# Kernel optimization log

Hardware: AMD Instinct MI355X
Metric: run time of the kernel (lower is better)

## Reference

```python
import jax, jax.numpy as jnp
from jax import lax
import numpy as np

B, C, L, HOP = 16, 64, 16384, 256
KS = 3        # LVC / conv kernel size
DIL = 3       # static Conv1d dilation (init arg)
KL = L // HOP # kernel_length (number of conditioning frames)


def setup_inputs() -> dict:
    key = jax.random.key(0)
    k0, k1, k2, k3 = jax.random.split(key, 4)
    return {
        "hidden_states": jax.random.normal(k0, (B, C, L), jnp.float32),
        "kernel": jax.random.normal(k1, (B, C, 2 * C, KS, KL), jnp.float32) * 0.05,
        "bias": jax.random.normal(k2, (B, 2 * C, KL), jnp.float32) * 0.05,
        "conv_w": jax.random.normal(k3, (C, C, KS), jnp.float32) * 0.05,
        "conv_b": jnp.zeros((C,), jnp.float32),
        "hop_size": HOP,
    }


def _lvc(x, kernel, bias, hop_size):
    # location-variable convolution; forward() uses dilation=1 here
    b, c, length = x.shape
    _, _, out_ch, ksize, klen = kernel.shape
    pad = (ksize - 1) // 2
    xp = jnp.pad(x, ((0, 0), (0, 0), (pad, pad)))
    # sliding windows of size ksize, stride 1 -> (b, c, length, ksize)
    win = jnp.stack([xp[:, :, i:i + length] for i in range(ksize)], axis=-1)
    # split time into (kernel_length, hop_size) frames
    win = win.reshape(b, c, klen, hop_size, ksize)
    # per-frame conv kernel contraction
    o = jnp.einsum('bilsk,biokl->bols', win, kernel)  # (b, out_ch, klen, hop)
    o = o + bias[:, :, :, None]
    return o.reshape(b, out_ch, klen * hop_size)


def reference(hidden_states, kernel, bias, conv_w, conv_b, hop_size):
    slope = 0.2
    pad = DIL * (KS - 1) // 2
    residual = hidden_states
    h = jax.nn.leaky_relu(hidden_states, slope)
    h = lax.conv_general_dilated(
        h, conv_w, window_strides=(1,), padding=[(pad, pad)],
        rhs_dilation=(DIL,), dimension_numbers=('NCH', 'OIH', 'NCH'))
    h = h + conv_b[None, :, None]
    h = jax.nn.leaky_relu(h, slope)
    h = _lvc(h, kernel, bias, hop_size)
    c = residual.shape[1]
    h = jax.nn.sigmoid(h[:, :c, :]) * jnp.tanh(h[:, c:, :])  # GLU gate
    return residual + h
```

## Files before the change

kernel.cpp:

```cpp
#include <hip/hip_runtime.h>
#include <hip/hip_bf16.h>

#define TB 256

typedef __attribute__((ext_vector_type(8))) short short8;
typedef __attribute__((ext_vector_type(4))) unsigned int uint4v;
typedef __attribute__((ext_vector_type(4))) float f32x4;

#define KTF_BYTES 50331648ull
#define WS_NEED   (KTF_BYTES + 24576ull)

static __device__ __forceinline__ float lrelu(float v){ return v > 0.f ? v : 0.2f*v; }

static __device__ __forceinline__ unsigned int pack2(float lo, float hi){
    __hip_bfloat162 h = __float22bfloat162_rn(float2{lo, hi});
    unsigned int r;
    __builtin_memcpy(&r, &h, 4);
    return r;
}

static __device__ __forceinline__ float bf2f(unsigned int u16v){
    return __uint_as_float(u16v << 16);
}

static __device__ __forceinline__ float glu_gate(float a, float t){
    float sg = 1.0f / (1.0f + __expf(-a));
    float e  = __expf(-2.0f * t);
    float th = 2.0f / (1.0f + e) - 1.0f;
    return sg * th;
}


__global__ __launch_bounds__(256, 4)
void ktf_transpose(const float* __restrict__ kern, unsigned int* __restrict__ ktf)
{
    __shared__ unsigned int tl32[128 * 65];
    const int tid = threadIdx.x;
    const int blk = blockIdx.x;
    const int k   = blk % 3;
    const int ci2 = (blk / 3) % 32;
    const int b   = blk / 96;
    const int kk  = k*2 + (ci2 >> 4);
    const int hi  = (ci2 >> 2) & 3;
    const int jp  = ci2 & 3;

    const float* src0 = kern + (size_t)b*1572864 + (size_t)ci2*49152 + k*64;
    #pragma unroll
    for (int it = 0; it < 8; ++it) {
        int p = tid + it*TB;
        int oc = p >> 4, fq = p & 15;
        const float* s = src0 + oc*192 + fq*4;
        float4 v0 = *(const float4*)(s);
        float4 v1 = *(const float4*)(s + 24576);
        unsigned int* d = tl32 + oc*65 + fq*4;
        d[0] = pack2(v0.x, v1.x);
        d[1] = pack2(v0.y, v1.y);
        d[2] = pack2(v0.z, v1.z);
        d[3] = pack2(v0.w, v1.w);
    }
    __syncthreads();

    const int l = tid & 63, wv = tid >> 6;
    const int mt = l >> 3, lo2 = (2*l) & 15;
    const size_t obase = (size_t)((kk*4 + jp)*8 + mt)*64 + hi*16 + lo2;
    #pragma unroll
    for (int fi = 0; fi < 16; ++fi) {
        int f = wv*16 + fi;
        uint2 v;
        v.x = tl32[(2*l    )*65 + f];
        v.y = tl32[(2*l + 1)*65 + f];
        *(uint2*)(ktf + (size_t)(b*64 + f)*12288 + obase) = v;
    }
}

__global__ __launch_bounds__(256, 4)
void wf_prep(const float* __restrict__ conv_w, unsigned int* __restrict__ wf)
{
    int u = blockIdx.x*TB + threadIdx.x;
    int ln = u & 63, mt = (u >> 6) & 3, jp = (u >> 8) & 3, kk = u >> 10;
    int lo = ln & 15, hi = ln >> 4;
    int m  = mt*16 + lo;
    int k  = kk >> 1, ci = (kk & 1)*32 + hi*8 + jp*2;
    float a0 = conv_w[m*192 + ci*3 + k];
    float a1 = conv_w[m*192 + (ci + 1)*3 + k];
    wf[u] = pack2(a0, a1);
}

#define LDS_BYTES (36864 + 34816 + 512)

__global__ __launch_bounds__(512, 4)
void fused_kernel(const float* __restrict__ x,
                  const float* __restrict__ bias,
                  const float* __restrict__ conv_b,
                  const unsigned int* __restrict__ ktf,
                  const unsigned int* __restrict__ wf,
                  float* __restrict__ out)
{
    __shared__ char lds[LDS_BYTES];
    float* bias_lds = (float*)(lds + 71680);

    const int tid = threadIdx.x;
    const int blk = blockIdx.x;
    const int b = blk >> 6, f = blk & 63;
    const int t0 = f << 8;
    const int ln = tid & 63, wv = tid >> 6;
    const int lo = ln & 15, hi = ln >> 4;
    const int mt = wv & 3, nth = wv >> 2;

    {
        const int g = wv;
        const float* xb = x + ((size_t)b*64 + g*8) * 16384;
        const bool interior = (f > 0) & (f < 63);
        #pragma unroll
        for (int it = 0; it < 5; ++it) {
            if (it < 4 || ln < 32) {
                int p = ln + it*64;
                int t = t0 - 12 + p;
                float v[8];
                if (interior) {
                    #pragma unroll
                    for (int j = 0; j < 8; ++j) v[j] = xb[j*16384 + t];
                } else {
                    bool ok = (unsigned)t < 16384u;
                    #pragma unroll
                    for (int j = 0; j < 8; ++j) v[j] = ok ? xb[j*16384 + t] : 0.f;
                }
                unsigned int w0 = pack2(lrelu(v[0]), lrelu(v[1]));
                unsigned int w1 = pack2(lrelu(v[2]), lrelu(v[3]));
                unsigned int w2 = pack2(lrelu(v[4]), lrelu(v[5]));
                unsigned int w3 = pack2(lrelu(v[6]), lrelu(v[7]));
                int addr = (p*128 + g*16) ^ ((p & 7) << 4);
                *(uint4*)(lds + addr) = make_uint4(w0, w1, w2, w3);
            }
        }
        if (tid < 128) bias_lds[tid] = bias[(size_t)b*8192 + tid*64 + f];
    }
    __syncthreads();

    {
        uint4v aw[6];
        #pragma unroll
        for (int kk = 0; kk < 6; ++kk) {
            int w0 = kk*1024 + mt*64 + ln;
            aw[kk].x = wf[w0      ]; aw[kk].y = wf[w0 + 256];
            aw[kk].z = wf[w0 + 512]; aw[kk].w = wf[w0 + 768];
        }
        float4 cb4 = *(const float4*)(conv_b + mt*16 + hi*4);
        const int n0  = nth ? 9 : 0;
        const int cnt = nth ? 8 : 9;
        #pragma unroll 1
        for (int i = 0; i < cnt; ++i) {
            int nt = n0 + i;
            short8 bq[6];
            #pragma unroll
            for (int kk = 0; kk < 6; ++kk) {
                int row = nt*16 + lo + 3*(kk >> 1) + 1;
                int cib = (kk & 1)*32 + hi*8;
                int addr = (row*128 + cib*2) ^ ((row & 7) << 4);
                bq[kk] = *(const short8*)(lds + addr);
            }
            f32x4 acc = {0.f, 0.f, 0.f, 0.f};
            __builtin_amdgcn_s_setprio(1);
            #pragma unroll
            for (int kk = 0; kk < 6; ++kk)
                acc = __builtin_amdgcn_mfma_f32_16x16x32_bf16(
                        __builtin_bit_cast(short8, aw[kk]), bq[kk], acc, 0, 0, 0);
            __builtin_amdgcn_s_setprio(0);

            int pos = t0 + nt*16 + lo - 8;
            bool valid = (unsigned)pos < 16384u;
            unsigned int h01 = valid ? pack2(lrelu(acc[0] + cb4.x), lrelu(acc[1] + cb4.y)) : 0u;
            unsigned int h23 = valid ? pack2(lrelu(acc[2] + cb4.z), lrelu(acc[3] + cb4.w)) : 0u;

            int htrow = nt*16 + lo;
            int addr = 36864 + ((htrow*128 + (mt*16 + hi*4)*2) ^ ((htrow & 7) << 4));
            unsigned int* d = (unsigned int*)(lds + addr);
            d[0] = h01; d[1] = h23;
        }
    }
    __syncthreads();

    {
        const unsigned int* kp = ktf + (size_t)blk * 12288;
        uint4v am0[6], am1[6];
        #pragma unroll
        for (int kk = 0; kk < 6; ++kk) {
            int b0 = kk*2048 + mt*64 + ln;
            am0[kk].x = kp[b0      ]; am0[kk].y = kp[b0 +  512];
            am0[kk].z = kp[b0 + 1024]; am0[kk].w = kp[b0 + 1536];
            int b1 = b0 + 256;
            am1[kk].x = kp[b1      ]; am1[kk].y = kp[b1 +  512];
            am1[kk].z = kp[b1 + 1024]; am1[kk].w = kp[b1 + 1536];
        }
        float ba[4], bb[4];
        size_t rowbase[4];
        #pragma unroll
        for (int r = 0; r < 4; ++r) {
            int c = mt*16 + hi*4 + r;
            ba[r] = bias_lds[c];
            bb[r] = bias_lds[c + 64];
            rowbase[r] = (size_t)(b*64 + c)*16384 + t0 + lo;
        }

        #pragma unroll 1
        for (int i = 0; i < 8; ++i) {
            int nt = nth*8 + i;
            int s = nt*16 + lo;
            short8 bq[6];
            #pragma unroll
            for (int kk = 0; kk < 6; ++kk) {
                int row = s + (kk >> 1) + 7;
                int cib = (kk & 1)*32 + hi*8;
                int addr = 36864 + ((row*128 + cib*2) ^ ((row & 7) << 4));
                bq[kk] = *(const short8*)(lds + addr);
            }
            int p = s + 12;
            int raddr = (p*128 + (mt*16 + hi*4)*2) ^ ((p & 7) << 4);
            uint2 rv = *(const uint2*)(lds + raddr);

            f32x4 a0 = {0.f,0.f,0.f,0.f}, a1 = {0.f,0.f,0.f,0.f};
            __builtin_amdgcn_s_setprio(1);
            #pragma unroll
            for (int kk = 0; kk < 6; ++kk) {
                a0 = __builtin_amdgcn_mfma_f32_16x16x32_bf16(
                        __builtin_bit_cast(short8, am0[kk]), bq[kk], a0, 0, 0, 0);
                a1 = __builtin_amdgcn_mfma_f32_16x16x32_bf16(
                        __builtin_bit_cast(short8, am1[kk]), bq[kk], a1, 0, 0, 0);
            }
            __builtin_amdgcn_s_setprio(0);

            #pragma unroll
            for (int r = 0; r < 4; ++r) {
                unsigned int u = (r < 2 ? rv.x : rv.y) >> ((r & 1) * 16);
                float hv = bf2f(u & 0xFFFFu);
                float xr = hv > 0.f ? hv : 5.0f * hv;
                float g  = glu_gate(a0[r] + ba[r], a1[r] + bb[r]);
                out[rowbase[r] + nt*16] = xr + g;
            }
        }
    }
}

extern "C" void kernel_launch(void* const* d_in, const int* in_sizes, int n_in,
                              void* d_out, int out_size, void* d_ws, size_t ws_size,
                              hipStream_t stream)
{
    const float* x      = (const float*)d_in[0];
    const float* kern   = (const float*)d_in[1];
    const float* bias   = (const float*)d_in[2];
    const float* conv_b = (const float*)d_in[4];
    float* out = (float*)d_out;

    if (ws_size < WS_NEED) return;

    unsigned int* ktf = (unsigned int*)d_ws;
    unsigned int* wf  = (unsigned int*)((char*)d_ws + KTF_BYTES);

    wf_prep      <<<dim3(24),   dim3(TB), 0, stream>>>((const float*)d_in[3], wf);
    ktf_transpose<<<dim3(1536), dim3(TB), 0, stream>>>(kern, ktf);
    fused_kernel <<<dim3(1024), dim3(512), 0, stream>>>(x, bias, conv_b, ktf, wf, out);
    (void)in_sizes; (void)n_in; (void)out_size;
}
```

Measured before the change: 90.52 us.

## Overlap x, weight and LVC kernel loads; vectorize x fetch; cheapen GLU gate

```diff
diff --git a/kernel.cpp b/kernel.cpp
--- a/kernel.cpp
+++ b/kernel.cpp
@@ -24,10 +24,11 @@
 }
 
 static __device__ __forceinline__ float glu_gate(float a, float t){
-    float sg = 1.0f / (1.0f + __expf(-a));
-    float e  = __expf(-2.0f * t);
-    float th = 2.0f / (1.0f + e) - 1.0f;
-    return sg * th;
+    t = fminf(fmaxf(t, -10.f), 10.f);
+    float u = __expf(-a);
+    float v = __expf(2.0f * t);
+    float den = (1.0f + u) * (v + 1.0f);
+    return (v - 1.0f) * __builtin_amdgcn_rcpf(den);
 }
 
 
@@ -107,82 +108,70 @@
     const int lo = ln & 15, hi = ln >> 4;
     const int mt = wv & 3, nth = wv >> 2;
 
+    const int g = wv;
+    const float* xb = x + ((size_t)b*64 + g*8) * 16384;
+    float2 xv[24];
     {
-        const int g = wv;
-        const float* xb = x + ((size_t)b*64 + g*8) * 16384;
         const bool interior = (f > 0) & (f < 63);
-        #pragma unroll
-        for (int it = 0; it < 5; ++it) {
-            if (it < 4 || ln < 32) {
-                int p = ln + it*64;
-                int t = t0 - 12 + p;
-                float v[8];
-                if (interior) {
+        if (interior) {
+            #pragma unroll
+            for (int it = 0; it < 3; ++it) {
+                if (it < 2 || ln < 16) {
+                    int t = t0 - 12 + 2*ln + it*128;
                     #pragma unroll
-                    for (int j = 0; j < 8; ++j) v[j] = xb[j*16384 + t];
-                } else {
-                    bool ok = (unsigned)t < 16384u;
+                    for (int j = 0; j < 8; ++j)
+                        xv[it*8 + j] = *(const float2*)(xb + j*16384 + t);
+                }
+            }
+        } else {
+            #pragma unroll
+            for (int it = 0; it < 3; ++it) {
+                if (it < 2 || ln < 16) {
+                    int t = t0 - 12 + 2*ln + it*128;
                     #pragma unroll
-                    for (int j = 0; j < 8; ++j) v[j] = ok ? xb[j*16384 + t] : 0.f;
+                    for (int j = 0; j < 8; ++j) {
+                        float a = ((unsigned)t       < 16384u) ? xb[j*16384 + t    ] : 0.f;
+                        float c = ((unsigned)(t + 1) < 16384u) ? xb[j*16384 + t + 1] : 0.f;
+                        xv[it*8 + j] = make_float2(a, c);
+                    }
                 }
-                unsigned int w0 = pack2(lrelu(v[0]), lrelu(v[1]));
-                unsigned int w1 = pack2(lrelu(v[2]), lrelu(v[3]));
-                unsigned int w2 = pack2(lrelu(v[4]), lrelu(v[5]));
-                unsigned int w3 = pack2(lrelu(v[6]), lrelu(v[7]));
-                int addr = (p*128 + g*16) ^ ((p & 7) << 4);
-                *(uint4*)(lds + addr) = make_uint4(w0, w1, w2, w3);
             }
         }
         if (tid < 128) bias_lds[tid] = bias[(size_t)b*8192 + tid*64 + f];
     }
-    __syncthreads();
-
-    {
-        uint4v aw[6];
-        #pragma unroll
-        for (int kk = 0; kk < 6; ++kk) {
-            int w0 = kk*1024 + mt*64 + ln;
-            aw[kk].x = wf[w0      ]; aw[kk].y = wf[w0 + 256];
-            aw[kk].z = wf[w0 + 512]; aw[kk].w = wf[w0 + 768];
-        }
-        float4 cb4 = *(const float4*)(conv_b + mt*16 + hi*4);
-        const int n0  = nth ? 9 : 0;
-        const int cnt = nth ? 8 : 9;
-        #pragma unroll 1
-        for (int i = 0; i < cnt; ++i) {
-            int nt = n0 + i;
-            short8 bq[6];
-            #pragma unroll
-            for (int kk = 0; kk < 6; ++kk) {
-                int row = nt*16 + lo + 3*(kk >> 1) + 1;
-                int cib = (kk & 1)*32 + hi*8;
-                int addr = (row*128 + cib*2) ^ ((row & 7) << 4);
-                bq[kk] = *(const short8*)(lds + addr);
-            }
-            f32x4 acc = {0.f, 0.f, 0.f, 0.f};
-            __builtin_amdgcn_s_setprio(1);
-            #pragma unroll
-            for (int kk = 0; kk < 6; ++kk)
-                acc = __builtin_amdgcn_mfma_f32_16x16x32_bf16(
-                        __builtin_bit_cast(short8, aw[kk]), bq[kk], acc, 0, 0, 0);
-            __builtin_amdgcn_s_setprio(0);
-
-            int pos = t0 + nt*16 + lo - 8;
-            bool valid = (unsigned)pos < 16384u;
-            unsigned int h01 = valid ? pack2(lrelu(acc[0] + cb4.x), lrelu(acc[1] + cb4.y)) : 0u;
-            unsigned int h23 = valid ? pack2(lrelu(acc[2] + cb4.z), lrelu(acc[3] + cb4.w)) : 0u;
-
-            int htrow = nt*16 + lo;
-            int addr = 36864 + ((htrow*128 + (mt*16 + hi*4)*2) ^ ((htrow & 7) << 4));
-            unsigned int* d = (unsigned int*)(lds + addr);
-            d[0] = h01; d[1] = h23;
-        }
-    }
-    __syncthreads();
-
+    __builtin_amdgcn_sched_barrier(0);
+
+    uint4v aw[6];
+    #pragma unroll
+    for (int kk = 0; kk < 6; ++kk) {
+        int w0 = kk*1024 + mt*64 + ln;
+        aw[kk].x = wf[w0      ]; aw[kk].y = wf[w0 + 256];
+        aw[kk].z = wf[w0 + 512]; aw[kk].w = wf[w0 + 768];
+    }
+    __builtin_amdgcn_sched_barrier(0);
+
+    #pragma unroll
+    for (int it = 0; it < 3; ++it) {
+        if (it < 2 || ln < 16) {
+            int p0 = 2*ln + it*128;
+            unsigned int w0[4], w1[4];
+            #pragma unroll
+            for (int jq = 0; jq < 4; ++jq) {
+                float2 e0 = xv[it*8 + 2*jq], e1 = xv[it*8 + 2*jq + 1];
+                w0[jq] = pack2(lrelu(e0.x), lrelu(e1.x));
+                w1[jq] = pack2(lrelu(e0.y), lrelu(e1.y));
+            }
+            int a0 = ( p0     *128 + g*16) ^ (( p0      & 7) << 4);
+            int a1 = ((p0 + 1)*128 + g*16) ^ (((p0 + 1) & 7) << 4);
+            *(uint4*)(lds + a0) = make_uint4(w0[0], w0[1], w0[2], w0[3]);
+            *(uint4*)(lds + a1) = make_uint4(w1[0], w1[1], w1[2], w1[3]);
+        }
+    }
+    __builtin_amdgcn_sched_barrier(0);
+
+    uint4v am0[6], am1[6];
     {
         const unsigned int* kp = ktf + (size_t)blk * 12288;
-        uint4v am0[6], am1[6];
         #pragma unroll
         for (int kk = 0; kk < 6; ++kk) {
             int b0 = kk*2048 + mt*64 + ln;
@@ -192,6 +181,50 @@
             am1[kk].x = kp[b1      ]; am1[kk].y = kp[b1 +  512];
             am1[kk].z = kp[b1 + 1024]; am1[kk].w = kp[b1 + 1536];
         }
+    }
+    __syncthreads();
+
+    {
+        float4 cb4 = *(const float4*)(conv_b + mt*16 + hi*4);
+        const int n0  = nth ? 9 : 0;
+        const int cnt = nth ? 8 : 9;
+        int bqa[6];
+        #pragma unroll
+        for (int kk = 0; kk < 6; ++kk) {
+            int row = n0*16 + lo + 3*(kk >> 1) + 1;
+            int cib = (kk & 1)*32 + hi*8;
+            bqa[kk] = (row*128 + cib*2) ^ ((row & 7) << 4);
+        }
+        int hta  = 36864 + (((n0*16 + lo)*128 + (mt*16 + hi*4)*2) ^ ((lo & 7) << 4));
+        int pos  = t0 + n0*16 + lo - 8;
+        #pragma unroll 1
+        for (int i = 0; i < cnt; ++i) {
+            short8 bq[6];
+            #pragma unroll
+            for (int kk = 0; kk < 6; ++kk)
+                bq[kk] = *(const short8*)(lds + bqa[kk]);
+            f32x4 acc = {0.f, 0.f, 0.f, 0.f};
+            __builtin_amdgcn_s_setprio(1);
+            #pragma unroll
+            for (int kk = 0; kk < 6; ++kk)
+                acc = __builtin_amdgcn_mfma_f32_16x16x32_bf16(
+                        __builtin_bit_cast(short8, aw[kk]), bq[kk], acc, 0, 0, 0);
+            __builtin_amdgcn_s_setprio(0);
+
+            bool valid = (unsigned)pos < 16384u;
+            unsigned int h01 = valid ? pack2(lrelu(acc[0] + cb4.x), lrelu(acc[1] + cb4.y)) : 0u;
+            unsigned int h23 = valid ? pack2(lrelu(acc[2] + cb4.z), lrelu(acc[3] + cb4.w)) : 0u;
+            unsigned int* d = (unsigned int*)(lds + hta);
+            d[0] = h01; d[1] = h23;
+
+            #pragma unroll
+            for (int kk = 0; kk < 6; ++kk) bqa[kk] += 2048;
+            hta += 2048; pos += 16;
+        }
+    }
+    __syncthreads();
+
+    {
         float ba[4], bb[4];
         size_t rowbase[4];
         #pragma unroll
@@ -199,24 +232,25 @@
             int c = mt*16 + hi*4 + r;
             ba[r] = bias_lds[c];
             bb[r] = bias_lds[c + 64];
-            rowbase[r] = (size_t)(b*64 + c)*16384 + t0 + lo;
-        }
+            rowbase[r] = (size_t)(b*64 + c)*16384 + t0 + nth*128 + lo;
+        }
+        int bqa[6];
+        #pragma unroll
+        for (int kk = 0; kk < 6; ++kk) {
+            int row = nth*128 + lo + (kk >> 1) + 7;
+            int cib = (kk & 1)*32 + hi*8;
+            bqa[kk] = 36864 + ((row*128 + cib*2) ^ ((row & 7) << 4));
+        }
+        int prow = nth*128 + lo + 12;
+        int ra   = (prow*128 + (mt*16 + hi*4)*2) ^ ((prow & 7) << 4);
 
         #pragma unroll 1
         for (int i = 0; i < 8; ++i) {
-            int nt = nth*8 + i;
-            int s = nt*16 + lo;
             short8 bq[6];
             #pragma unroll
-            for (int kk = 0; kk < 6; ++kk) {
-                int row = s + (kk >> 1) + 7;
-                int cib = (kk & 1)*32 + hi*8;
-                int addr = 36864 + ((row*128 + cib*2) ^ ((row & 7) << 4));
-                bq[kk] = *(const short8*)(lds + addr);
-            }
-            int p = s + 12;
-            int raddr = (p*128 + (mt*16 + hi*4)*2) ^ ((p & 7) << 4);
-            uint2 rv = *(const uint2*)(lds + raddr);
+            for (int kk = 0; kk < 6; ++kk)
+                bq[kk] = *(const short8*)(lds + bqa[kk]);
+            uint2 rv = *(const uint2*)(lds + ra);
 
             f32x4 a0 = {0.f,0.f,0.f,0.f}, a1 = {0.f,0.f,0.f,0.f};
             __builtin_amdgcn_s_setprio(1);
@@ -234,9 +268,12 @@
                 unsigned int u = (r < 2 ? rv.x : rv.y) >> ((r & 1) * 16);
                 float hv = bf2f(u & 0xFFFFu);
                 float xr = hv > 0.f ? hv : 5.0f * hv;
-                float g  = glu_gate(a0[r] + ba[r], a1[r] + bb[r]);
-                out[rowbase[r] + nt*16] = xr + g;
-            }
+                float gg = glu_gate(a0[r] + ba[r], a1[r] + bb[r]);
+                out[rowbase[r] + (size_t)i*16] = xr + gg;
+            }
+            #pragma unroll
+            for (int kk = 0; kk < 6; ++kk) bqa[kk] += 2048;
+            ra += 2048;
         }
     }
 }
```

New measurement: 84.29 us. -6.9%, faster.

## Split frame into two halves, shrink LDS, repack LVC kernel per wave

Applied to the files above, without the earlier changes.

```diff
diff --git a/kernel.cpp b/kernel.cpp
--- a/kernel.cpp
+++ b/kernel.cpp
@@ -24,10 +24,11 @@
 }
 
 static __device__ __forceinline__ float glu_gate(float a, float t){
-    float sg = 1.0f / (1.0f + __expf(-a));
-    float e  = __expf(-2.0f * t);
-    float th = 2.0f / (1.0f + e) - 1.0f;
-    return sg * th;
+    t = fminf(fmaxf(t, -10.f), 10.f);
+    float u = __expf(-a);
+    float v = __expf(2.0f * t);
+    float den = (1.0f + u) * (v + 1.0f);
+    return (v - 1.0f) * __builtin_amdgcn_rcpf(den);
 }
 
 
@@ -60,16 +61,20 @@
     }
     __syncthreads();
 
-    const int l = tid & 63, wv = tid >> 6;
-    const int mt = l >> 3, lo2 = (2*l) & 15;
-    const size_t obase = (size_t)((kk*4 + jp)*8 + mt)*64 + hi*16 + lo2;
+    const int l = tid & 63, wvv = tid >> 6;
+    const int c = (kk*4 + jp)*4 + hi;
+    const int oc0 = 2*l;
+    const int slot0 = (oc0 < 64) ? ((oc0 >> 3)*16 + (oc0 & 7))
+                                 : (((oc0 - 64) >> 3)*16 + 8 + ((oc0 - 64) & 7));
+    unsigned int* dst = ktf + (size_t)(b*96 + c)*8192 + slot0;
+    const int f0 = wvv*16;
     #pragma unroll
     for (int fi = 0; fi < 16; ++fi) {
-        int f = wv*16 + fi;
+        int f = f0 + fi;
         uint2 v;
-        v.x = tl32[(2*l    )*65 + f];
-        v.y = tl32[(2*l + 1)*65 + f];
-        *(uint2*)(ktf + (size_t)(b*64 + f)*12288 + obase) = v;
+        v.x = tl32[(oc0    )*65 + f];
+        v.y = tl32[(oc0 + 1)*65 + f];
+        *(uint2*)(dst + f*128) = v;
     }
 }
 
@@ -86,9 +91,10 @@
     wf[u] = pack2(a0, a1);
 }
 
-#define LDS_BYTES (36864 + 34816 + 512)
-
-__global__ __launch_bounds__(512, 4)
+#define LDS_HT   18432
+#define LDS_BIAS 36864
+
+__global__ __launch_bounds__(512, 8)
 void fused_kernel(const float* __restrict__ x,
                   const float* __restrict__ bias,
                   const float* __restrict__ conv_b,
@@ -96,8 +102,8 @@
                   const unsigned int* __restrict__ wf,
                   float* __restrict__ out)
 {
-    __shared__ char lds[LDS_BYTES];
-    float* bias_lds = (float*)(lds + 71680);
+    __shared__ char lds[37376];
+    float* bias_lds = (float*)(lds + LDS_BIAS);
 
     const int tid = threadIdx.x;
     const int blk = blockIdx.x;
@@ -107,135 +113,147 @@
     const int lo = ln & 15, hi = ln >> 4;
     const int mt = wv & 3, nth = wv >> 2;
 
-    {
-        const int g = wv;
-        const float* xb = x + ((size_t)b*64 + g*8) * 16384;
-        const bool interior = (f > 0) & (f < 63);
-        #pragma unroll
-        for (int it = 0; it < 5; ++it) {
-            if (it < 4 || ln < 32) {
-                int p = ln + it*64;
-                int t = t0 - 12 + p;
-                float v[8];
-                if (interior) {
-                    #pragma unroll
-                    for (int j = 0; j < 8; ++j) v[j] = xb[j*16384 + t];
-                } else {
-                    bool ok = (unsigned)t < 16384u;
-                    #pragma unroll
-                    for (int j = 0; j < 8; ++j) v[j] = ok ? xb[j*16384 + t] : 0.f;
+    if (tid < 128) bias_lds[tid] = bias[(size_t)b*8192 + tid*64 + f];
+
+    const float* xb = x + ((size_t)b*64 + wv*8) * 16384;
+
+    #pragma unroll 1
+    for (int h = 0; h < 2; ++h) {
+        if (h) __syncthreads();
+
+        {
+            const int tb = t0 + h*128 - 12;
+            const bool interior = (tb >= 0) & (tb + 143 < 16384);
+            #pragma unroll
+            for (int it = 0; it < 3; ++it) {
+                int p = (it < 2) ? (ln + it*64) : (128 + ln);
+                if (it < 2 || ln < 16) {
+                    int t = tb + p;
+                    float v[8];
+                    if (interior) {
+                        #pragma unroll
+                        for (int j = 0; j < 8; ++j) v[j] = xb[j*16384 + t];
+                    } else {
+                        bool ok = (unsigned)t < 16384u;
+                        #pragma unroll
+                        for (int j = 0; j < 8; ++j) v[j] = ok ? xb[j*16384 + t] : 0.f;
+                    }
+                    unsigned int w0 = pack2(lrelu(v[0]), lrelu(v[1]));
+                    unsigned int w1 = pack2(lrelu(v[2]), lrelu(v[3]));
+                    unsigned int w2 = pack2(lrelu(v[4]), lrelu(v[5]));
+                    unsigned int w3 = pack2(lrelu(v[6]), lrelu(v[7]));
+                    int a = (p*128 + wv*16) ^ ((p & 7) << 4);
+                    *(uint4*)(lds + a) = make_uint4(w0, w1, w2, w3);
                 }
-                unsigned int w0 = pack2(lrelu(v[0]), lrelu(v[1]));
-                unsigned int w1 = pack2(lrelu(v[2]), lrelu(v[3]));
-                unsigned int w2 = pack2(lrelu(v[4]), lrelu(v[5]));
-                unsigned int w3 = pack2(lrelu(v[6]), lrelu(v[7]));
-                int addr = (p*128 + g*16) ^ ((p & 7) << 4);
-                *(uint4*)(lds + addr) = make_uint4(w0, w1, w2, w3);
             }
         }
-        if (tid < 128) bias_lds[tid] = bias[(size_t)b*8192 + tid*64 + f];
-    }
-    __syncthreads();
-
-    {
-        uint4v aw[6];
-        #pragma unroll
-        for (int kk = 0; kk < 6; ++kk) {
-            int w0 = kk*1024 + mt*64 + ln;
-            aw[kk].x = wf[w0      ]; aw[kk].y = wf[w0 + 256];
-            aw[kk].z = wf[w0 + 512]; aw[kk].w = wf[w0 + 768];
+        __syncthreads();
+
+        {
+            uint4v aw[6];
+            #pragma unroll
+            for (int kk = 0; kk < 6; ++kk) {
+                int w0 = kk*1024 + mt*64 + ln;
+                aw[kk].x = wf[w0      ]; aw[kk].y = wf[w0 + 256];
+                aw[kk].z = wf[w0 + 512]; aw[kk].w = wf[w0 + 768];
+            }
+            float4 cb4 = *(const float4*)(conv_b + mt*16 + hi*4);
+            const int n0  = nth ? 5 : 0;
+            const int cnt = nth ? 4 : 5;
+            int bqa[6];
+            #pragma unroll
+            for (int kk = 0; kk < 6; ++kk) {
+                int row = n0*16 + lo + 3*(kk >> 1) + 1;
+                int cib = (kk & 1)*32 + hi*8;
+                bqa[kk] = (row*128 + cib*2) ^ ((row & 7) << 4);
+            }
+            int hta = LDS_HT + (((n0*16 + lo)*128 + (mt*16 + hi*4)*2) ^ ((lo & 7) << 4));
+            int pos = t0 + h*128 + n0*16 + lo - 8;
+            #pragma unroll 1
+            for (int i = 0; i < cnt; ++i) {
+                f32x4 acc = {0.f, 0.f, 0.f, 0.f};
+                __builtin_amdgcn_s_setprio(1);
+                #pragma unroll
+                for (int kk = 0; kk < 6; ++kk) {
+                    short8 bq = *(const short8*)(lds + bqa[kk]);
+                    acc = __builtin_amdgcn_mfma_f32_16x16x32_bf16(
+                            __builtin_bit_cast(short8, aw[kk]), bq, acc, 0, 0, 0);
+                }
+                __builtin_amdgcn_s_setprio(0);
+
+                bool valid = (unsigned)pos < 16384u;
+                unsigned int h01 = valid ? pack2(lrelu(acc[0] + cb4.x), lrelu(acc[1] + cb4.y)) : 0u;
+                unsigned int h23 = valid ? pack2(lrelu(acc[2] + cb4.z), lrelu(acc[3] + cb4.w)) : 0u;
+                unsigned int* d = (unsigned int*)(lds + hta);
+                d[0] = h01; d[1] = h23;
+
+                #pragma unroll
+                for (int kk = 0; kk < 6; ++kk) bqa[kk] += 2048;
+                hta += 2048; pos += 16;
+            }
         }
-        float4 cb4 = *(const float4*)(conv_b + mt*16 + hi*4);
-        const int n0  = nth ? 9 : 0;
-        const int cnt = nth ? 8 : 9;
-        #pragma unroll 1
-        for (int i = 0; i < cnt; ++i) {
-            int nt = n0 + i;
-            short8 bq[6];
-            #pragma unroll
-            for (int kk = 0; kk < 6; ++kk) {
-                int row = nt*16 + lo + 3*(kk >> 1) + 1;
+        __syncthreads();
+
+        {
+            uint4v am[6];
+            const unsigned int* kp = ktf + (size_t)b*786432 + hi*8192 + f*128 + wv*16 + lo;
+            #pragma unroll
+            for (int kk = 0; kk < 6; ++kk) {
+                int o = kk*131072;
+                am[kk].x = kp[o        ]; am[kk].y = kp[o + 32768];
+                am[kk].z = kp[o + 65536]; am[kk].w = kp[o + 98304];
+            }
+            const int c0 = wv*8;
+            const bool alane = hi < 2;
+            const int chA = alane ? (c0 + hi*4) : (c0 + (hi - 2)*4 + 2);
+            float bs0 = bias_lds[chA],      bs1 = bias_lds[chA + 1];
+            float bt0 = bias_lds[chA + 64], bt1 = bias_lds[chA + 65];
+
+            int bqa[6];
+            #pragma unroll
+            for (int kk = 0; kk < 6; ++kk) {
+                int row = lo + 7 + (kk >> 1);
                 int cib = (kk & 1)*32 + hi*8;
-                int addr = (row*128 + cib*2) ^ ((row & 7) << 4);
-                bq[kk] = *(const short8*)(lds + addr);
-            }
-            f32x4 acc = {0.f, 0.f, 0.f, 0.f};
-            __builtin_amdgcn_s_setprio(1);
-            #pragma unroll
-            for (int kk = 0; kk < 6; ++kk)
-                acc = __builtin_amdgcn_mfma_f32_16x16x32_bf16(
-                        __builtin_bit_cast(short8, aw[kk]), bq[kk], acc, 0, 0, 0);
-            __builtin_amdgcn_s_setprio(0);
-
-            int pos = t0 + nt*16 + lo - 8;
-            bool valid = (unsigned)pos < 16384u;
-            unsigned int h01 = valid ? pack2(lrelu(acc[0] + cb4.x), lrelu(acc[1] + cb4.y)) : 0u;
-            unsigned int h23 = valid ? pack2(lrelu(acc[2] + cb4.z), lrelu(acc[3] + cb4.w)) : 0u;
-
-            int htrow = nt*16 + lo;
-            int addr = 36864 + ((htrow*128 + (mt*16 + hi*4)*2) ^ ((htrow & 7) << 4));
-            unsigned int* d = (unsigned int*)(lds + addr);
-            d[0] = h01; d[1] = h23;
-        }
-    }
-    __syncthreads();
-
-    {
-        const unsigned int* kp = ktf + (size_t)blk * 12288;
-        uint4v am0[6], am1[6];
-        #pragma unroll
-        for (int kk = 0; kk < 6; ++kk) {
-            int b0 = kk*2048 + mt*64 + ln;
-            am0[kk].x = kp[b0      ]; am0[kk].y = kp[b0 +  512];
-            am0[kk].z = kp[b0 + 1024]; am0[kk].w = kp[b0 + 1536];
-            int b1 = b0 + 256;
-            am1[kk].x = kp[b1      ]; am1[kk].y = kp[b1 +  512];
-            am1[kk].z = kp[b1 + 1024]; am1[kk].w = kp[b1 + 1536];
-        }
-        float ba[4], bb[4];
-        size_t rowbase[4];
-        #pragma unroll
-        for (int r = 0; r < 4; ++r) {
-            int c = mt*16 + hi*4 + r;
-            ba[r] = bias_lds[c];
-            bb[r] = bias_lds[c + 64];
-            rowbase[r] = (size_t)(b*64 + c)*16384 + t0 + lo;
-        }
-
-        #pragma unroll 1
-        for (int i = 0; i < 8; ++i) {
-            int nt = nth*8 + i;
-            int s = nt*16 + lo;
-            short8 bq[6];
-            #pragma unroll
-            for (int kk = 0; kk < 6; ++kk) {
-                int row = s + (kk >> 1) + 7;
-                int cib = (kk & 1)*32 + hi*8;
-                int addr = 36864 + ((row*128 + cib*2) ^ ((row & 7) << 4));
-                bq[kk] = *(const short8*)(lds + addr);
-            }
-            int p = s + 12;
-            int raddr = (p*128 + (mt*16 + hi*4)*2) ^ ((p & 7) << 4);
-            uint2 rv = *(const uint2*)(lds + raddr);
-
-            f32x4 a0 = {0.f,0.f,0.f,0.f}, a1 = {0.f,0.f,0.f,0.f};
-            __builtin_amdgcn_s_setprio(1);
-            #pragma unroll
-            for (int kk = 0; kk < 6; ++kk) {
-                a0 = __builtin_amdgcn_mfma_f32_16x16x32_bf16(
-                        __builtin_bit_cast(short8, am0[kk]), bq[kk], a0, 0, 0, 0);
-                a1 = __builtin_amdgcn_mfma_f32_16x16x32_bf16(
-                        __builtin_bit_cast(short8, am1[kk]), bq[kk], a1, 0, 0, 0);
-            }
-            __builtin_amdgcn_s_setprio(0);
-
-            #pragma unroll
-            for (int r = 0; r < 4; ++r) {
-                unsigned int u = (r < 2 ? rv.x : rv.y) >> ((r & 1) * 16);
-                float hv = bf2f(u & 0xFFFFu);
-                float xr = hv > 0.f ? hv : 5.0f * hv;
-                float g  = glu_gate(a0[r] + ba[r], a1[r] + bb[r]);
-                out[rowbase[r] + nt*16] = xr + g;
+                bqa[kk] = LDS_HT + ((row*128 + cib*2) ^ ((row & 7) << 4));
+            }
+            int q  = lo + 12;
+            int ra = (q*128 + chA*2) ^ ((q & 7) << 4);
+            float* ob = out + ((size_t)b*64 + chA)*16384 + t0 + h*128 + lo;
+
+            #pragma unroll 1
+            for (int i = 0; i < 8; ++i) {
+                f32x4 acc = {0.f, 0.f, 0.f, 0.f};
+                __builtin_amdgcn_s_setprio(1);
+                #pragma unroll
+                for (int kk = 0; kk < 6; ++kk) {
+                    short8 bq = *(const short8*)(lds + bqa[kk]);
+                    acc = __builtin_amdgcn_mfma_f32_16x16x32_bf16(
+                            __builtin_bit_cast(short8, am[kk]), bq, acc, 0, 0, 0);
+                }
+                __builtin_amdgcn_s_setprio(0);
+
+                float q1 = alane ? acc[2] : acc[0];
+                float q2 = alane ? acc[3] : acc[1];
+                float r1 = __shfl_xor(q1, 32, 64);
+                float r2 = __shfl_xor(q2, 32, 64);
+                float sig0 = alane ? acc[0] : r1;
+                float tan0 = alane ? r1 : acc[2];
+                float sig1 = alane ? acc[1] : r2;
+                float tan1 = alane ? r2 : acc[3];
+
+                unsigned int rv = *(const unsigned int*)(lds + ra);
+                float h0 = bf2f(rv & 0xFFFFu), h1 = bf2f(rv >> 16);
+                float xr0 = h0 > 0.f ? h0 : 5.0f*h0;
+                float xr1 = h1 > 0.f ? h1 : 5.0f*h1;
+
+                float g0 = glu_gate(sig0 + bs0, tan0 + bt0);
+                float g1 = glu_gate(sig1 + bs1, tan1 + bt1);
+                ob[(size_t)i*16]           = xr0 + g0;
+                ob[16384 + (size_t)i*16]   = xr1 + g1;
+
+                #pragma unroll
+                for (int kk = 0; kk < 6; ++kk) bqa[kk] += 2048;
+                ra += 2048;
             }
         }
     }
```

After: 151.7 us. +67.6%, slower.
